# Performance work log

Measured on AMD Instinct MI355X. Metric: run time of the kernel, lower is better.

## Reference

```python
import jax, jax.numpy as jnp
import numpy as np


def log_g(x):
    # log of g(x) = where(x>=0, x+0.5, sigmoid(x))
    return jnp.where(x >= 0, jnp.log(jnp.maximum(x, 0.0) + 0.5), -jax.nn.softplus(-x))


def setup_inputs() -> dict:
    key = jax.random.key(0)
    k1, k2 = jax.random.split(key)
    B, S, D = 8, 8192, 512
    x = jax.random.normal(k1, (B, S, D), dtype=jnp.float32)
    # to_hidden_and_gate weight: [2*D, D] (orthogonal init in torch; gaussian ok for reference)
    W = jax.random.normal(k2, (2 * D, D), dtype=jnp.float32) / np.sqrt(D)
    return {"x": x, "W": W}


def reference(x, W):
    # x: [B, S, D], W: [2D, D]
    hg = jnp.einsum('bsd,ed->bse', x, W)  # [B, S, 2D]
    D = x.shape[-1]
    hidden, gate = hg[..., :D], hg[..., D:]

    # log-domain minGRU (Heinsen associative scan)
    log_coeffs = -jax.nn.softplus(gate)            # log(1 - z)
    log_z = -jax.nn.softplus(-gate)                # log(z)
    log_values = log_z + log_g(hidden)             # log(z * g(h~))

    a_star = jnp.cumsum(log_coeffs, axis=1)
    log_h = a_star + jax.lax.cumlogsumexp(log_values - a_star, axis=1)
    out = jnp.exp(log_h)                           # [B, S, D]

    next_prev_hidden = out[:, -1:]
    return out, next_prev_hidden
```

## Files before the change

kernel.cpp:

```cpp
#include <hip/hip_runtime.h>
#include <hip/hip_bf16.h>
#include <stdint.h>

typedef float f32x4 __attribute__((ext_vector_type(4)));
typedef __bf16 bf16x8 __attribute__((ext_vector_type(8)));
typedef unsigned short ushort8 __attribute__((ext_vector_type(8)));

#define NB 8
#define NS 8192
#define ND 512
#define NM (NB * NS)
#define NK 512

__device__ __forceinline__ unsigned short f2bf(float f) {
  unsigned u = __float_as_uint(f);
  u += 0x7FFFu + ((u >> 16) & 1u);
  return (unsigned short)(u >> 16);
}

__global__ __launch_bounds__(256) void cvt_bf16(const float* __restrict__ src,
                                                unsigned short* __restrict__ dst,
                                                int n8) {
  int i = blockIdx.x * 256 + threadIdx.x;
  if (i >= n8) return;
  const float4* s = reinterpret_cast<const float4*>(src + (size_t)i * 8);
  float4 v0 = s[0], v1 = s[1];
  ushort8 o;
  o[0] = f2bf(v0.x); o[1] = f2bf(v0.y); o[2] = f2bf(v0.z); o[3] = f2bf(v0.w);
  o[4] = f2bf(v1.x); o[5] = f2bf(v1.y); o[6] = f2bf(v1.z); o[7] = f2bf(v1.w);
  *reinterpret_cast<ushort8*>(dst + (size_t)i * 8) = o;
}

__global__ __launch_bounds__(256) void gemm_ab(const unsigned short* __restrict__ xb,
                                               const unsigned short* __restrict__ wb,
                                               uint32_t* __restrict__ pk,
                                               float* __restrict__ aggA,
                                               float* __restrict__ aggB) {
  __shared__ __align__(16) unsigned short lds[2 * 16384];
  __shared__ float aggL[128];

  const int tid = threadIdx.x;
  const int w = tid >> 6;
  const int lane = tid & 63;
  const int wr = w >> 1;
  const int wc = w & 1;
  const int orig = blockIdx.x;
  const int wg = (orig & 7) * 512 + (orig >> 3);
  const int mblk = wg >> 3;
  const int nblk = wg & 7;
  const int m0 = mblk * 128;
  const int n0 = nblk * 64;

  const int lrow = lane >> 3;
  const int lcol = (((lane & 7) ^ lrow) * 8);

  const unsigned short* pA[4];
  const unsigned short* pB[4];
#pragma unroll
  for (int i = 0; i < 4; ++i) {
    int row = i * 32 + w * 8 + lrow;
    pA[i] = xb + (size_t)(m0 + row) * NK + lcol;
    int e = (row < 64) ? (n0 + row) : (448 + n0 + row);
    pB[i] = wb + (size_t)e * NK + lcol;
  }

  auto stage = [&](int buf, int kt) {
    unsigned short* base = lds + buf * 16384;
    const int ko = kt << 6;
#pragma unroll
    for (int i = 0; i < 4; ++i) {
      __builtin_amdgcn_global_load_lds(
          (const __attribute__((address_space(1))) void*)(pA[i] + ko),
          (__attribute__((address_space(3))) void*)(base + i * 2048 + w * 512),
          16, 0, 0);
      __builtin_amdgcn_global_load_lds(
          (const __attribute__((address_space(1))) void*)(pB[i] + ko),
          (__attribute__((address_space(3))) void*)(base + 8192 + i * 2048 + w * 512),
          16, 0, 0);
    }
  };

  f32x4 acc[4][4];
#pragma unroll
  for (int i = 0; i < 4; ++i)
#pragma unroll
    for (int j = 0; j < 4; ++j) acc[i][j] = (f32x4)0.0f;

  const int fr = lane & 15;
  const int kg = lane >> 4;

  stage(0, 0);
  __syncthreads();

#pragma unroll 1
  for (int kt = 0; kt < 8; ++kt) {
    const int cur = kt & 1;
    if (kt < 7) stage(cur ^ 1, kt + 1);

    const char* ldsA = (const char*)(lds + cur * 16384);
    const char* ldsB = ldsA + 16384;
#pragma unroll
    for (int kk = 0; kk < 64; kk += 32) {
      bf16x8 af[4], bfr[4];
#pragma unroll
      for (int i = 0; i < 4; ++i) {
        int rowA = wr * 64 + i * 16 + fr;
        int swzA = (kk * 2 + kg * 16) ^ ((rowA & 7) << 4);
        af[i] = *reinterpret_cast<const bf16x8*>(ldsA + rowA * 128 + swzA);
        int rowB = ((i < 2) ? (wc * 32 + i * 16) : (64 + wc * 32 + (i - 2) * 16)) + fr;
        int swzB = (kk * 2 + kg * 16) ^ ((rowB & 7) << 4);
        bfr[i] = *reinterpret_cast<const bf16x8*>(ldsB + rowB * 128 + swzB);
      }
#pragma unroll
      for (int i = 0; i < 4; ++i)
#pragma unroll
        for (int j = 0; j < 4; ++j)
          acc[i][j] = __builtin_amdgcn_mfma_f32_16x16x32_bf16(af[i], bfr[j], acc[i][j], 0, 0, 0);
    }
    __syncthreads();
  }

  const float LOG2E = 1.44269504f;
  float A64[2], B64[2];
#pragma unroll
  for (int n = 0; n < 2; ++n) {
    const int ch = wc * 32 + n * 16 + fr;
    float Am[4], Bm[4];
#pragma unroll
    for (int m = 0; m < 4; ++m) {
      float As = 1.0f, Bs = 0.0f;
#pragma unroll
      for (int r = 0; r < 4; ++r) {
        float hid = acc[m][n][r];
        float gat = acc[m][n + 2][r];
        float ex1 = __builtin_amdgcn_exp2f(gat * LOG2E);
        float a = __builtin_amdgcn_rcpf(1.0f + ex1);
        float z = 1.0f - a;
        float ex2 = __builtin_amdgcn_exp2f(-hid * LOG2E);
        float gn = __builtin_amdgcn_rcpf(1.0f + ex2);
        float g = (hid >= 0.0f) ? (hid + 0.5f) : gn;
        float bb = z * g;
        int row = 64 * wr + 16 * m + 4 * kg + r;
        pk[(size_t)(m0 + row) * ND + n0 + ch] =
            ((uint32_t)f2bf(bb) << 16) | (uint32_t)f2bf(a);
        Bs = fmaf(a, Bs, bb);
        As *= a;
      }
      Am[m] = As; Bm[m] = Bs;
    }
#pragma unroll
    for (int m = 0; m < 4; ++m) {
      float pA_ = __shfl_xor(Am[m], 16);
      float pB_ = __shfl_xor(Bm[m], 16);
      Bm[m] = (kg & 1) ? fmaf(Am[m], pB_, Bm[m]) : fmaf(pA_, Bm[m], pB_);
      Am[m] *= pA_;
      pA_ = __shfl_xor(Am[m], 32);
      pB_ = __shfl_xor(Bm[m], 32);
      Bm[m] = (kg & 2) ? fmaf(Am[m], pB_, Bm[m]) : fmaf(pA_, Bm[m], pB_);
      Am[m] *= pA_;
    }
    float As = Am[0], Bs = Bm[0];
#pragma unroll
    for (int m = 1; m < 4; ++m) { Bs = fmaf(Am[m], Bs, Bm[m]); As *= Am[m]; }
    A64[n] = As; B64[n] = Bs;
  }
  if (wr == 0 && kg == 0) {
#pragma unroll
    for (int n = 0; n < 2; ++n) {
      int ch = wc * 32 + n * 16 + fr;
      aggL[ch * 2] = A64[n];
      aggL[ch * 2 + 1] = B64[n];
    }
  }
  __syncthreads();
  if (wr == 1 && kg == 0) {
#pragma unroll
    for (int n = 0; n < 2; ++n) {
      int ch = wc * 32 + n * 16 + fr;
      float A0 = aggL[ch * 2], B0 = aggL[ch * 2 + 1];
      size_t o = (size_t)mblk * ND + n0 + ch;
      aggA[o] = A0 * A64[n];
      aggB[o] = fmaf(A64[n], B0, B64[n]);
    }
  }
}

__global__ __launch_bounds__(256) void scan_pass2(const uint32_t* __restrict__ pk,
                                                  const float* __restrict__ aggA,
                                                  const float* __restrict__ aggB,
                                                  float* __restrict__ out,
                                                  float* __restrict__ nextp) {
  int bid = blockIdx.x;
  int b = bid >> 6;
  int c = bid & 63;
  int d2 = threadIdx.x;

  float h0 = 0.0f, h1 = 0.0f;
  for (int cc = 0; cc < c; ++cc) {
    int o = (b * 64 + cc) * ND + d2 * 2;
    float2 Aa = *reinterpret_cast<const float2*>(&aggA[o]);
    float2 Bb = *reinterpret_cast<const float2*>(&aggB[o]);
    h0 = fmaf(Aa.x, h0, Bb.x);
    h1 = fmaf(Aa.y, h1, Bb.y);
  }
  size_t base = (size_t)(b * NS + c * 128) * ND + d2 * 2;
#pragma unroll 4
  for (int t = 0; t < 128; ++t) {
    size_t idx = base + (size_t)t * ND;
    uint2 v = *reinterpret_cast<const uint2*>(pk + idx);
    float a0 = __uint_as_float(v.x << 16);
    float b0 = __uint_as_float(v.x & 0xffff0000u);
    float a1 = __uint_as_float(v.y << 16);
    float b1 = __uint_as_float(v.y & 0xffff0000u);
    h0 = fmaf(a0, h0, b0);
    h1 = fmaf(a1, h1, b1);
    *reinterpret_cast<float2*>(&out[idx]) = make_float2(h0, h1);
  }
  if (c == 63) {
    *reinterpret_cast<float2*>(&nextp[b * ND + d2 * 2]) = make_float2(h0, h1);
  }
}

extern "C" void kernel_launch(void* const* d_in, const int* in_sizes, int n_in,
                              void* d_out, int out_size, void* d_ws, size_t ws_size,
                              hipStream_t stream) {
  const float* x = (const float*)d_in[0];
  const float* W = (const float*)d_in[1];
  float* out = (float*)d_out;

  char* ws = (char*)d_ws;
  unsigned short* xb  = (unsigned short*)ws;
  unsigned short* wbf = (unsigned short*)(ws + (size_t)64 * 1024 * 1024);
  uint32_t* pk = (uint32_t*)(ws + (size_t)65 * 1024 * 1024);
  float* aggA = (float*)(ws + (size_t)193 * 1024 * 1024);
  float* aggB = (float*)(ws + (size_t)194 * 1024 * 1024);
  float* nextp = out + (size_t)NM * ND;

  cvt_bf16<<<16384, 256, 0, stream>>>(x, xb, (NM * NK) / 8);
  cvt_bf16<<<256, 256, 0, stream>>>(W, wbf, (1024 * NK) / 8);
  gemm_ab<<<4096, 256, 0, stream>>>(xb, wbf, pk, aggA, aggB);
  scan_pass2<<<512, 256, 0, stream>>>(pk, aggA, aggB, out, nextp);
}
```

Baseline: 231.4 us.

## Fuse fp32-to-bf16 conversion of x into GEMM LDS load path

```diff
diff --git a/kernel.cpp b/kernel.cpp
--- a/kernel.cpp
+++ b/kernel.cpp
@@ -16,6 +16,12 @@
   unsigned u = __float_as_uint(f);
   u += 0x7FFFu + ((u >> 16) & 1u);
   return (unsigned short)(u >> 16);
+}
+
+__device__ __forceinline__ uint32_t cvtpk(float lo, float hi) {
+  uint32_t r;
+  asm("v_cvt_pk_bf16_f32 %0, %1, %2" : "=v"(r) : "v"(lo), "v"(hi));
+  return r;
 }
 
 __global__ __launch_bounds__(256) void cvt_bf16(const float* __restrict__ src,
@@ -31,12 +37,12 @@
   *reinterpret_cast<ushort8*>(dst + (size_t)i * 8) = o;
 }
 
-__global__ __launch_bounds__(256) void gemm_ab(const unsigned short* __restrict__ xb,
+__global__ __launch_bounds__(256) void gemm_ab(const float* __restrict__ x,
                                                const unsigned short* __restrict__ wb,
                                                uint32_t* __restrict__ pk,
                                                float* __restrict__ aggA,
                                                float* __restrict__ aggB) {
-  __shared__ __align__(16) unsigned short lds[2 * 16384];
+  __shared__ __align__(16) char lds[2 * 24576];
   __shared__ float aggL[128];
 
   const int tid = threadIdx.x;
@@ -51,33 +57,37 @@
   const int m0 = mblk * 128;
   const int n0 = nblk * 64;
 
-  const int lrow = lane >> 3;
-  const int lcol = (((lane & 7) ^ lrow) * 8);
-
-  const unsigned short* pA[4];
-  const unsigned short* pB[4];
-#pragma unroll
-  for (int i = 0; i < 4; ++i) {
-    int row = i * 32 + w * 8 + lrow;
-    pA[i] = xb + (size_t)(m0 + row) * NK + lcol;
+  const int aSrc = (((lane & 7) ^ (lane >> 3)) << 2);
+  const float* pAf[4];
+#pragma unroll
+  for (int g = 0; g < 4; ++g) {
+    int row = g * 32 + w * 8 + (lane >> 3);
+    pAf[g] = x + (size_t)(m0 + row) * NK + aSrc;
+  }
+  const int bSrc = (((lane & 3) ^ ((lane >> 2) & 3)) << 3);
+  const unsigned short* pBf[2];
+#pragma unroll
+  for (int g = 0; g < 2; ++g) {
+    int row = g * 64 + w * 16 + (lane >> 2);
     int e = (row < 64) ? (n0 + row) : (448 + n0 + row);
-    pB[i] = wb + (size_t)e * NK + lcol;
+    pBf[g] = wb + (size_t)e * NK + bSrc;
   }
 
   auto stage = [&](int buf, int kt) {
-    unsigned short* base = lds + buf * 16384;
-    const int ko = kt << 6;
-#pragma unroll
-    for (int i = 0; i < 4; ++i) {
+    char* base = lds + buf * 24576;
+    const int ko = kt << 5;
+#pragma unroll
+    for (int g = 0; g < 4; ++g)
       __builtin_amdgcn_global_load_lds(
-          (const __attribute__((address_space(1))) void*)(pA[i] + ko),
-          (__attribute__((address_space(3))) void*)(base + i * 2048 + w * 512),
+          (const __attribute__((address_space(1))) void*)(pAf[g] + ko),
+          (__attribute__((address_space(3))) void*)(base + (g * 4 + w) * 1024),
           16, 0, 0);
+#pragma unroll
+    for (int g = 0; g < 2; ++g)
       __builtin_amdgcn_global_load_lds(
-          (const __attribute__((address_space(1))) void*)(pB[i] + ko),
-          (__attribute__((address_space(3))) void*)(base + 8192 + i * 2048 + w * 512),
+          (const __attribute__((address_space(1))) void*)(pBf[g] + ko),
+          (__attribute__((address_space(3))) void*)(base + 16384 + (g * 4 + w) * 1024),
           16, 0, 0);
-    }
   };
 
   f32x4 acc[4][4];
@@ -93,30 +103,35 @@
   __syncthreads();
 
 #pragma unroll 1
-  for (int kt = 0; kt < 8; ++kt) {
+  for (int kt = 0; kt < 16; ++kt) {
     const int cur = kt & 1;
-    if (kt < 7) stage(cur ^ 1, kt + 1);
-
-    const char* ldsA = (const char*)(lds + cur * 16384);
+    if (kt < 15) stage(cur ^ 1, kt + 1);
+
+    const char* ldsA = lds + cur * 24576;
     const char* ldsB = ldsA + 16384;
-#pragma unroll
-    for (int kk = 0; kk < 64; kk += 32) {
-      bf16x8 af[4], bfr[4];
-#pragma unroll
-      for (int i = 0; i < 4; ++i) {
-        int rowA = wr * 64 + i * 16 + fr;
-        int swzA = (kk * 2 + kg * 16) ^ ((rowA & 7) << 4);
-        af[i] = *reinterpret_cast<const bf16x8*>(ldsA + rowA * 128 + swzA);
-        int rowB = ((i < 2) ? (wc * 32 + i * 16) : (64 + wc * 32 + (i - 2) * 16)) + fr;
-        int swzB = (kk * 2 + kg * 16) ^ ((rowB & 7) << 4);
-        bfr[i] = *reinterpret_cast<const bf16x8*>(ldsB + rowB * 128 + swzB);
-      }
-#pragma unroll
-      for (int i = 0; i < 4; ++i)
-#pragma unroll
-        for (int j = 0; j < 4; ++j)
-          acc[i][j] = __builtin_amdgcn_mfma_f32_16x16x32_bf16(af[i], bfr[j], acc[i][j], 0, 0, 0);
-    }
+    bf16x8 af[4], bfr[4];
+#pragma unroll
+    for (int i = 0; i < 4; ++i) {
+      int rowA = wr * 64 + i * 16 + fr;
+      int s0 = ((2 * kg) ^ (fr & 7)) << 4;
+      int s1 = ((2 * kg + 1) ^ (fr & 7)) << 4;
+      f32x4 q0 = *reinterpret_cast<const f32x4*>(ldsA + rowA * 128 + s0);
+      f32x4 q1 = *reinterpret_cast<const f32x4*>(ldsA + rowA * 128 + s1);
+      uint4 u;
+      u.x = cvtpk(q0[0], q0[1]);
+      u.y = cvtpk(q0[2], q0[3]);
+      u.z = cvtpk(q1[0], q1[1]);
+      u.w = cvtpk(q1[2], q1[3]);
+      af[i] = *reinterpret_cast<bf16x8*>(&u);
+      int rowB = ((i < 2) ? (wc * 32 + i * 16) : (64 + wc * 32 + (i - 2) * 16)) + fr;
+      bfr[i] = *reinterpret_cast<const bf16x8*>(ldsB + rowB * 64 + ((kg ^ (fr & 3)) << 4));
+    }
+#pragma unroll
+    for (int i = 0; i < 4; ++i)
+#pragma unroll
+      for (int j = 0; j < 4; ++j)
+        acc[i][j] = __builtin_amdgcn_mfma_f32_16x16x32_bf16(af[i], bfr[j], acc[i][j], 0, 0, 0);
+
     __syncthreads();
   }
 
@@ -229,15 +244,13 @@
   float* out = (float*)d_out;
 
   char* ws = (char*)d_ws;
-  unsigned short* xb  = (unsigned short*)ws;
-  unsigned short* wbf = (unsigned short*)(ws + (size_t)64 * 1024 * 1024);
-  uint32_t* pk = (uint32_t*)(ws + (size_t)65 * 1024 * 1024);
-  float* aggA = (float*)(ws + (size_t)193 * 1024 * 1024);
-  float* aggB = (float*)(ws + (size_t)194 * 1024 * 1024);
+  uint32_t* pk = (uint32_t*)ws;
+  unsigned short* wbf = (unsigned short*)(ws + (size_t)128 * 1024 * 1024);
+  float* aggA = (float*)(ws + (size_t)129 * 1024 * 1024);
+  float* aggB = (float*)(ws + (size_t)130 * 1024 * 1024);
   float* nextp = out + (size_t)NM * ND;
 
-  cvt_bf16<<<16384, 256, 0, stream>>>(x, xb, (NM * NK) / 8);
   cvt_bf16<<<256, 256, 0, stream>>>(W, wbf, (1024 * NK) / 8);
-  gemm_ab<<<4096, 256, 0, stream>>>(xb, wbf, pk, aggA, aggB);
+  gemm_ab<<<4096, 256, 0, stream>>>(x, wbf, pk, aggA, aggB);
   scan_pass2<<<512, 256, 0, stream>>>(pk, aggA, aggB, out, nextp);
 }
```

New measurement: 230.5 us. Within noise of the previous version (-0.4%).

## Enlarge GEMM tile to 256 rows with 8 waves and triple-buffered LDS pipeline

Applied to the files above, without the earlier changes.

```diff
diff --git a/kernel.cpp b/kernel.cpp
--- a/kernel.cpp
+++ b/kernel.cpp
@@ -31,13 +31,13 @@
   *reinterpret_cast<ushort8*>(dst + (size_t)i * 8) = o;
 }
 
-__global__ __launch_bounds__(256) void gemm_ab(const unsigned short* __restrict__ xb,
+__global__ __launch_bounds__(512) void gemm_ab(const unsigned short* __restrict__ xb,
                                                const unsigned short* __restrict__ wb,
                                                uint32_t* __restrict__ pk,
                                                float* __restrict__ aggA,
                                                float* __restrict__ aggB) {
-  __shared__ __align__(16) unsigned short lds[2 * 16384];
-  __shared__ float aggL[128];
+  __shared__ __align__(16) char lds[3 * 49152];
+  __shared__ float aggL[256];
 
   const int tid = threadIdx.x;
   const int w = tid >> 6;
@@ -45,80 +45,128 @@
   const int wr = w >> 1;
   const int wc = w & 1;
   const int orig = blockIdx.x;
-  const int wg = (orig & 7) * 512 + (orig >> 3);
+  const int wg = (orig & 7) * 256 + (orig >> 3);
   const int mblk = wg >> 3;
   const int nblk = wg & 7;
-  const int m0 = mblk * 128;
+  const int m0 = mblk * 256;
   const int n0 = nblk * 64;
 
   const int lrow = lane >> 3;
   const int lcol = (((lane & 7) ^ lrow) * 8);
 
   const unsigned short* pA[4];
-  const unsigned short* pB[4];
-#pragma unroll
-  for (int i = 0; i < 4; ++i) {
-    int row = i * 32 + w * 8 + lrow;
-    pA[i] = xb + (size_t)(m0 + row) * NK + lcol;
+#pragma unroll
+  for (int g = 0; g < 4; ++g) {
+    int row = g * 64 + w * 8 + lrow;
+    pA[g] = xb + (size_t)(m0 + row) * NK + lcol;
+  }
+  const unsigned short* pB[2];
+#pragma unroll
+  for (int g = 0; g < 2; ++g) {
+    int row = g * 64 + w * 8 + lrow;
     int e = (row < 64) ? (n0 + row) : (448 + n0 + row);
-    pB[i] = wb + (size_t)e * NK + lcol;
-  }
-
-  auto stage = [&](int buf, int kt) {
-    unsigned short* base = lds + buf * 16384;
-    const int ko = kt << 6;
-#pragma unroll
-    for (int i = 0; i < 4; ++i) {
-      __builtin_amdgcn_global_load_lds(
-          (const __attribute__((address_space(1))) void*)(pA[i] + ko),
-          (__attribute__((address_space(3))) void*)(base + i * 2048 + w * 512),
-          16, 0, 0);
-      __builtin_amdgcn_global_load_lds(
-          (const __attribute__((address_space(1))) void*)(pB[i] + ko),
-          (__attribute__((address_space(3))) void*)(base + 8192 + i * 2048 + w * 512),
-          16, 0, 0);
-    }
-  };
-
-  f32x4 acc[4][4];
-#pragma unroll
-  for (int i = 0; i < 4; ++i)
-#pragma unroll
-    for (int j = 0; j < 4; ++j) acc[i][j] = (f32x4)0.0f;
+    pB[g] = wb + (size_t)e * NK + lcol;
+  }
 
   const int fr = lane & 15;
   const int kg = lane >> 4;
 
-  stage(0, 0);
-  __syncthreads();
-
-#pragma unroll 1
-  for (int kt = 0; kt < 8; ++kt) {
-    const int cur = kt & 1;
-    if (kt < 7) stage(cur ^ 1, kt + 1);
-
-    const char* ldsA = (const char*)(lds + cur * 16384);
-    const char* ldsB = ldsA + 16384;
-#pragma unroll
-    for (int kk = 0; kk < 64; kk += 32) {
-      bf16x8 af[4], bfr[4];
-#pragma unroll
-      for (int i = 0; i < 4; ++i) {
-        int rowA = wr * 64 + i * 16 + fr;
-        int swzA = (kk * 2 + kg * 16) ^ ((rowA & 7) << 4);
-        af[i] = *reinterpret_cast<const bf16x8*>(ldsA + rowA * 128 + swzA);
-        int rowB = ((i < 2) ? (wc * 32 + i * 16) : (64 + wc * 32 + (i - 2) * 16)) + fr;
-        int swzB = (kk * 2 + kg * 16) ^ ((rowB & 7) << 4);
-        bfr[i] = *reinterpret_cast<const bf16x8*>(ldsB + rowB * 128 + swzB);
-      }
-#pragma unroll
-      for (int i = 0; i < 4; ++i)
-#pragma unroll
-        for (int j = 0; j < 4; ++j)
-          acc[i][j] = __builtin_amdgcn_mfma_f32_16x16x32_bf16(af[i], bfr[j], acc[i][j], 0, 0, 0);
-    }
-    __syncthreads();
-  }
+  f32x4 acc[4][4];
+#pragma unroll
+  for (int i = 0; i < 4; ++i)
+#pragma unroll
+    for (int j = 0; j < 4; ++j) acc[i][j] = (f32x4)0.0f;
+
+  bf16x8 af[4], bfr[4];
+
+#define GLD(SRC, DSTOFF)                                                      \
+  __builtin_amdgcn_global_load_lds(                                           \
+      (const __attribute__((address_space(1))) void*)(SRC),                   \
+      (__attribute__((address_space(3))) void*)(lds + (DSTOFF)), 16, 0, 0)
+
+#define STG1(S, KT)                                                           \
+  {                                                                           \
+    GLD(pA[0] + (KT) * 64, (S) * 49152 + (0 * 8 + w) * 1024);                 \
+    GLD(pA[1] + (KT) * 64, (S) * 49152 + (1 * 8 + w) * 1024);                 \
+    GLD(pA[2] + (KT) * 64, (S) * 49152 + (2 * 8 + w) * 1024);                 \
+  }
+#define STG2(S, KT)                                                           \
+  {                                                                           \
+    GLD(pA[3] + (KT) * 64, (S) * 49152 + (3 * 8 + w) * 1024);                 \
+    GLD(pB[0] + (KT) * 64, (S) * 49152 + 32768 + (0 * 8 + w) * 1024);         \
+    GLD(pB[1] + (KT) * 64, (S) * 49152 + 32768 + (1 * 8 + w) * 1024);         \
+  }
+
+#define READF(C, KK)                                                          \
+  {                                                                           \
+    const char* ldsA_ = lds + (C) * 49152;                                    \
+    const char* ldsB_ = ldsA_ + 32768;                                        \
+    _Pragma("unroll")                                                         \
+    for (int i = 0; i < 4; ++i) {                                             \
+      int rowA = wr * 64 + i * 16 + fr;                                       \
+      int sa = ((KK) * 2 + kg * 16) ^ ((rowA & 7) << 4);                      \
+      af[i] = *reinterpret_cast<const bf16x8*>(ldsA_ + rowA * 128 + sa);      \
+      int rowB = ((i < 2) ? (wc * 32 + i * 16) : (64 + wc * 32 + (i - 2) * 16)) + fr; \
+      int sb = ((KK) * 2 + kg * 16) ^ ((rowB & 7) << 4);                      \
+      bfr[i] = *reinterpret_cast<const bf16x8*>(ldsB_ + rowB * 128 + sb);     \
+    }                                                                         \
+  }
+
+#define MFMA16()                                                              \
+  {                                                                           \
+    _Pragma("unroll")                                                         \
+    for (int i = 0; i < 4; ++i)                                               \
+      _Pragma("unroll")                                                       \
+      for (int j = 0; j < 4; ++j)                                             \
+        acc[i][j] = __builtin_amdgcn_mfma_f32_16x16x32_bf16(af[i], bfr[j],    \
+                                                            acc[i][j], 0, 0, 0); \
+  }
+
+#define BAR() __builtin_amdgcn_s_barrier()
+#define SB0() __builtin_amdgcn_sched_barrier(0)
+#define LGKM0() asm volatile("s_waitcnt lgkmcnt(0)" ::: "memory")
+#define VMC(N) asm volatile("s_waitcnt vmcnt(" #N ")" ::: "memory")
+
+#define ITER(KT, C, S, DO, WMODE)                                             \
+  {                                                                           \
+    READF(C, 0);                                                              \
+    if (DO) STG1(S, (KT) + 2);                                                \
+    BAR(); LGKM0(); SB0();                                                    \
+    __builtin_amdgcn_s_setprio(1); MFMA16(); __builtin_amdgcn_s_setprio(0);   \
+    BAR();                                                                    \
+    READF(C, 32);                                                             \
+    if (DO) STG2(S, (KT) + 2);                                                \
+    BAR(); LGKM0(); SB0();                                                    \
+    __builtin_amdgcn_s_setprio(1); MFMA16(); __builtin_amdgcn_s_setprio(0);   \
+    if (WMODE == 1) { VMC(6); SB0(); }                                        \
+    if (WMODE == 2) { VMC(0); SB0(); }                                        \
+    BAR();                                                                    \
+  }
+
+  STG1(0, 0); STG2(0, 0);
+  STG1(1, 1); STG2(1, 1);
+  VMC(6); SB0();
+  BAR();
+
+  ITER(0, 0, 2, 1, 1);
+  ITER(1, 1, 0, 1, 1);
+  ITER(2, 2, 1, 1, 1);
+  ITER(3, 0, 2, 1, 1);
+  ITER(4, 1, 0, 1, 1);
+  ITER(5, 2, 1, 1, 1);
+  ITER(6, 0, 2, 0, 2);
+  ITER(7, 1, 0, 0, 0);
+
+#undef ITER
+#undef GLD
+#undef STG1
+#undef STG2
+#undef READF
+#undef MFMA16
+#undef BAR
+#undef SB0
+#undef LGKM0
+#undef VMC
 
   const float LOG2E = 1.44269504f;
   float A64[2], B64[2];
@@ -140,7 +188,7 @@
         float gn = __builtin_amdgcn_rcpf(1.0f + ex2);
         float g = (hid >= 0.0f) ? (hid + 0.5f) : gn;
         float bb = z * g;
-        int row = 64 * wr + 16 * m + 4 * kg + r;
+        int row = wr * 64 + 16 * m + 4 * kg + r;
         pk[(size_t)(m0 + row) * ND + n0 + ch] =
             ((uint32_t)f2bf(bb) << 16) | (uint32_t)f2bf(a);
         Bs = fmaf(a, Bs, bb);
@@ -164,21 +212,22 @@
     for (int m = 1; m < 4; ++m) { Bs = fmaf(Am[m], Bs, Bm[m]); As *= Am[m]; }
     A64[n] = As; B64[n] = Bs;
   }
-  if (wr == 0 && kg == 0) {
+  if ((wr & 1) == 0 && kg == 0) {
 #pragma unroll
     for (int n = 0; n < 2; ++n) {
       int ch = wc * 32 + n * 16 + fr;
-      aggL[ch * 2] = A64[n];
-      aggL[ch * 2 + 1] = B64[n];
+      aggL[(wr >> 1) * 128 + ch * 2] = A64[n];
+      aggL[(wr >> 1) * 128 + ch * 2 + 1] = B64[n];
     }
   }
   __syncthreads();
-  if (wr == 1 && kg == 0) {
+  if ((wr & 1) == 1 && kg == 0) {
 #pragma unroll
     for (int n = 0; n < 2; ++n) {
       int ch = wc * 32 + n * 16 + fr;
-      float A0 = aggL[ch * 2], B0 = aggL[ch * 2 + 1];
-      size_t o = (size_t)mblk * ND + n0 + ch;
+      float A0 = aggL[(wr >> 1) * 128 + ch * 2];
+      float B0 = aggL[(wr >> 1) * 128 + ch * 2 + 1];
+      size_t o = (size_t)(mblk * 2 + (wr >> 1)) * ND + n0 + ch;
       aggA[o] = A0 * A64[n];
       aggB[o] = fmaf(A64[n], B0, B64[n]);
     }
@@ -238,6 +287,6 @@
 
   cvt_bf16<<<16384, 256, 0, stream>>>(x, xb, (NM * NK) / 8);
   cvt_bf16<<<256, 256, 0, stream>>>(W, wbf, (1024 * NK) / 8);
-  gemm_ab<<<4096, 256, 0, stream>>>(xb, wbf, pk, aggA, aggB);
+  gemm_ab<<<2048, 512, 0, stream>>>(xb, wbf, pk, aggA, aggB);
   scan_pass2<<<512, 256, 0, stream>>>(pk, aggA, aggB, out, nextp);
 }
```

Result: slower. 236.8 us (+2.4%).

## Enlarge GEMM tile to 256x128 with 8 waves per block

Applied to the files above, without the earlier changes.

```diff
diff --git a/kernel.cpp b/kernel.cpp
--- a/kernel.cpp
+++ b/kernel.cpp
@@ -31,25 +31,24 @@
   *reinterpret_cast<ushort8*>(dst + (size_t)i * 8) = o;
 }
 
-__global__ __launch_bounds__(256) void gemm_ab(const unsigned short* __restrict__ xb,
-                                               const unsigned short* __restrict__ wb,
-                                               uint32_t* __restrict__ pk,
-                                               float* __restrict__ aggA,
-                                               float* __restrict__ aggB) {
-  __shared__ __align__(16) unsigned short lds[2 * 16384];
-  __shared__ float aggL[128];
+__global__ __launch_bounds__(512, 2) void gemm_ab(const unsigned short* __restrict__ xb,
+                                                  const unsigned short* __restrict__ wb,
+                                                  uint32_t* __restrict__ pk,
+                                                  float* __restrict__ aggA,
+                                                  float* __restrict__ aggB) {
+  __shared__ __align__(16) char lds[2 * 65536];
 
   const int tid = threadIdx.x;
   const int w = tid >> 6;
   const int lane = tid & 63;
-  const int wr = w >> 1;
-  const int wc = w & 1;
+  const int wm = w >> 2;
+  const int wn = w & 3;
   const int orig = blockIdx.x;
-  const int wg = (orig & 7) * 512 + (orig >> 3);
-  const int mblk = wg >> 3;
-  const int nblk = wg & 7;
-  const int m0 = mblk * 128;
-  const int n0 = nblk * 64;
+  const int wg = (orig & 7) * 128 + (orig >> 3);
+  const int mblk = wg >> 2;
+  const int nblk = wg & 3;
+  const int m0 = mblk * 256;
+  const int n0 = nblk * 128;
 
   const int lrow = lane >> 3;
   const int lcol = (((lane & 7) ^ lrow) * 8);
@@ -57,37 +56,37 @@
   const unsigned short* pA[4];
   const unsigned short* pB[4];
 #pragma unroll
-  for (int i = 0; i < 4; ++i) {
-    int row = i * 32 + w * 8 + lrow;
-    pA[i] = xb + (size_t)(m0 + row) * NK + lcol;
-    int e = (row < 64) ? (n0 + row) : (448 + n0 + row);
-    pB[i] = wb + (size_t)e * NK + lcol;
+  for (int g = 0; g < 4; ++g) {
+    int row = g * 64 + w * 8 + lrow;
+    pA[g] = xb + (size_t)(m0 + row) * NK + lcol;
+    int e = (row < 128) ? (n0 + row) : (384 + n0 + row);
+    pB[g] = wb + (size_t)e * NK + lcol;
   }
 
   auto stage = [&](int buf, int kt) {
-    unsigned short* base = lds + buf * 16384;
+    char* base = lds + buf * 65536;
     const int ko = kt << 6;
 #pragma unroll
-    for (int i = 0; i < 4; ++i) {
+    for (int g = 0; g < 4; ++g) {
       __builtin_amdgcn_global_load_lds(
-          (const __attribute__((address_space(1))) void*)(pA[i] + ko),
-          (__attribute__((address_space(3))) void*)(base + i * 2048 + w * 512),
+          (const __attribute__((address_space(1))) void*)(pA[g] + ko),
+          (__attribute__((address_space(3))) void*)(base + g * 8192 + w * 1024),
           16, 0, 0);
       __builtin_amdgcn_global_load_lds(
-          (const __attribute__((address_space(1))) void*)(pB[i] + ko),
-          (__attribute__((address_space(3))) void*)(base + 8192 + i * 2048 + w * 512),
+          (const __attribute__((address_space(1))) void*)(pB[g] + ko),
+          (__attribute__((address_space(3))) void*)(base + 32768 + g * 8192 + w * 1024),
           16, 0, 0);
     }
   };
-
-  f32x4 acc[4][4];
-#pragma unroll
-  for (int i = 0; i < 4; ++i)
-#pragma unroll
-    for (int j = 0; j < 4; ++j) acc[i][j] = (f32x4)0.0f;
 
   const int fr = lane & 15;
   const int kg = lane >> 4;
+
+  f32x4 acc[8][4];
+#pragma unroll
+  for (int i = 0; i < 8; ++i)
+#pragma unroll
+    for (int j = 0; j < 4; ++j) acc[i][j] = (f32x4)0.0f;
 
   stage(0, 0);
   __syncthreads();
@@ -97,22 +96,25 @@
     const int cur = kt & 1;
     if (kt < 7) stage(cur ^ 1, kt + 1);
 
-    const char* ldsA = (const char*)(lds + cur * 16384);
-    const char* ldsB = ldsA + 16384;
+    const char* ldsA = lds + cur * 65536;
+    const char* ldsB = ldsA + 32768;
 #pragma unroll
     for (int kk = 0; kk < 64; kk += 32) {
-      bf16x8 af[4], bfr[4];
-#pragma unroll
-      for (int i = 0; i < 4; ++i) {
-        int rowA = wr * 64 + i * 16 + fr;
-        int swzA = (kk * 2 + kg * 16) ^ ((rowA & 7) << 4);
-        af[i] = *reinterpret_cast<const bf16x8*>(ldsA + rowA * 128 + swzA);
-        int rowB = ((i < 2) ? (wc * 32 + i * 16) : (64 + wc * 32 + (i - 2) * 16)) + fr;
-        int swzB = (kk * 2 + kg * 16) ^ ((rowB & 7) << 4);
-        bfr[i] = *reinterpret_cast<const bf16x8*>(ldsB + rowB * 128 + swzB);
+      bf16x8 af[8], bfr[4];
+#pragma unroll
+      for (int i = 0; i < 8; ++i) {
+        int rowA = wm * 128 + i * 16 + fr;
+        int sa = (kk * 2 + kg * 16) ^ ((rowA & 7) << 4);
+        af[i] = *reinterpret_cast<const bf16x8*>(ldsA + rowA * 128 + sa);
       }
 #pragma unroll
-      for (int i = 0; i < 4; ++i)
+      for (int n = 0; n < 4; ++n) {
+        int rowB = ((n < 2) ? (wn * 32 + n * 16) : (128 + wn * 32 + (n - 2) * 16)) + fr;
+        int sb = (kk * 2 + kg * 16) ^ ((rowB & 7) << 4);
+        bfr[n] = *reinterpret_cast<const bf16x8*>(ldsB + rowB * 128 + sb);
+      }
+#pragma unroll
+      for (int i = 0; i < 8; ++i)
 #pragma unroll
         for (int j = 0; j < 4; ++j)
           acc[i][j] = __builtin_amdgcn_mfma_f32_16x16x32_bf16(af[i], bfr[j], acc[i][j], 0, 0, 0);
@@ -121,13 +123,12 @@
   }
 
   const float LOG2E = 1.44269504f;
-  float A64[2], B64[2];
 #pragma unroll
   for (int n = 0; n < 2; ++n) {
-    const int ch = wc * 32 + n * 16 + fr;
-    float Am[4], Bm[4];
-#pragma unroll
-    for (int m = 0; m < 4; ++m) {
+    const int ch = wn * 32 + n * 16 + fr;
+    float Am[8], Bm[8];
+#pragma unroll
+    for (int m = 0; m < 8; ++m) {
       float As = 1.0f, Bs = 0.0f;
 #pragma unroll
       for (int r = 0; r < 4; ++r) {
@@ -140,7 +141,7 @@
         float gn = __builtin_amdgcn_rcpf(1.0f + ex2);
         float g = (hid >= 0.0f) ? (hid + 0.5f) : gn;
         float bb = z * g;
-        int row = 64 * wr + 16 * m + 4 * kg + r;
+        int row = wm * 128 + 16 * m + 4 * kg + r;
         pk[(size_t)(m0 + row) * ND + n0 + ch] =
             ((uint32_t)f2bf(bb) << 16) | (uint32_t)f2bf(a);
         Bs = fmaf(a, Bs, bb);
@@ -149,7 +150,7 @@
       Am[m] = As; Bm[m] = Bs;
     }
 #pragma unroll
-    for (int m = 0; m < 4; ++m) {
+    for (int m = 0; m < 8; ++m) {
       float pA_ = __shfl_xor(Am[m], 16);
       float pB_ = __shfl_xor(Bm[m], 16);
       Bm[m] = (kg & 1) ? fmaf(Am[m], pB_, Bm[m]) : fmaf(pA_, Bm[m], pB_);
@@ -161,26 +162,11 @@
     }
     float As = Am[0], Bs = Bm[0];
 #pragma unroll
-    for (int m = 1; m < 4; ++m) { Bs = fmaf(Am[m], Bs, Bm[m]); As *= Am[m]; }
-    A64[n] = As; B64[n] = Bs;
-  }
-  if (wr == 0 && kg == 0) {
-#pragma unroll
-    for (int n = 0; n < 2; ++n) {
-      int ch = wc * 32 + n * 16 + fr;
-      aggL[ch * 2] = A64[n];
-      aggL[ch * 2 + 1] = B64[n];
-    }
-  }
-  __syncthreads();
-  if (wr == 1 && kg == 0) {
-#pragma unroll
-    for (int n = 0; n < 2; ++n) {
-      int ch = wc * 32 + n * 16 + fr;
-      float A0 = aggL[ch * 2], B0 = aggL[ch * 2 + 1];
-      size_t o = (size_t)mblk * ND + n0 + ch;
-      aggA[o] = A0 * A64[n];
-      aggB[o] = fmaf(A64[n], B0, B64[n]);
+    for (int m = 1; m < 8; ++m) { Bs = fmaf(Am[m], Bs, Bm[m]); As *= Am[m]; }
+    if (kg == 0) {
+      size_t o = (size_t)(mblk * 2 + wm) * ND + n0 + ch;
+      aggA[o] = As;
+      aggB[o] = Bs;
     }
   }
 }
@@ -238,6 +224,6 @@
 
   cvt_bf16<<<16384, 256, 0, stream>>>(x, xb, (NM * NK) / 8);
   cvt_bf16<<<256, 256, 0, stream>>>(W, wbf, (1024 * NK) / 8);
-  gemm_ab<<<4096, 256, 0, stream>>>(xb, wbf, pk, aggA, aggB);
+  gemm_ab<<<1024, 512, 0, stream>>>(xb, wbf, pk, aggA, aggB);
   scan_pass2<<<512, 256, 0, stream>>>(pk, aggA, aggB, out, nextp);
 }
```

After: 225.1 us. 2.7% less time.
